# Optimization experiments

Hardware: AMD Instinct MI355X
Metric: run time of the kernel (lower is better)

The kernel has to match this reference:

```python
import jax, jax.numpy as jnp
import numpy as np

NUM_NODES = 50000
NUM_EDGES = 800000
INPUT_DIM = 128
HIDDEN_DIM = 128
PE_DIM = 64


def setup_inputs() -> dict:
    key = jax.random.key(0)
    ks = jax.random.split(key, 12)
    x = jax.random.normal(ks[0], (NUM_NODES, INPUT_DIM), dtype=jnp.float32)
    edge_index = jax.random.randint(ks[1], (2, NUM_EDGES), 0, NUM_NODES, dtype=jnp.int64)
    edge_pe = jax.random.normal(ks[2], (NUM_EDGES, PE_DIM), dtype=jnp.float32)
    # message_net: Linear(input+pe -> hidden), ReLU, Linear(hidden -> hidden)
    s1 = 1.0 / np.sqrt(INPUT_DIM + PE_DIM)
    W1 = jax.random.uniform(ks[3], (INPUT_DIM + PE_DIM, HIDDEN_DIM), minval=-s1, maxval=s1)
    b1 = jax.random.uniform(ks[4], (HIDDEN_DIM,), minval=-s1, maxval=s1)
    s2 = 1.0 / np.sqrt(HIDDEN_DIM)
    W2 = jax.random.uniform(ks[5], (HIDDEN_DIM, HIDDEN_DIM), minval=-s2, maxval=s2)
    b2 = jax.random.uniform(ks[6], (HIDDEN_DIM,), minval=-s2, maxval=s2)
    # update_net: Linear(input+hidden -> hidden), ReLU, Linear(hidden -> input)
    s3 = 1.0 / np.sqrt(INPUT_DIM + HIDDEN_DIM)
    U1 = jax.random.uniform(ks[7], (INPUT_DIM + HIDDEN_DIM, HIDDEN_DIM), minval=-s3, maxval=s3)
    c1 = jax.random.uniform(ks[8], (HIDDEN_DIM,), minval=-s3, maxval=s3)
    U2 = jax.random.uniform(ks[9], (HIDDEN_DIM, INPUT_DIM), minval=-s2, maxval=s2)
    c2 = jax.random.uniform(ks[10], (INPUT_DIM,), minval=-s2, maxval=s2)
    return {"x": x, "edge_pe": edge_pe, "W1": W1, "b1": b1, "W2": W2, "b2": b2,
            "U1": U1, "c1": c1, "U2": U2, "c2": c2, "edge_index": edge_index}


def reference(x, edge_pe, W1, b1, W2, b2, U1, c1, U2, c2, edge_index):
    src, dst = edge_index[0], edge_index[1]
    # gather source node features per edge: [E, input_dim]
    msg_in = jnp.concatenate([x[src], edge_pe], axis=-1)  # [E, input+pe]
    h = jax.nn.relu(msg_in @ W1 + b1)
    messages = h @ W2 + b2  # [E, hidden]
    # scatter-add messages to destination nodes
    aggregated = jax.ops.segment_sum(messages, dst, num_segments=x.shape[0])  # [N, hidden]
    upd_in = jnp.concatenate([x, aggregated], axis=-1)  # [N, input+hidden]
    u = jax.nn.relu(upd_in @ U1 + c1)
    return u @ U2 + c2  # [N, input_dim]
```

## Files before the change

kernel.cpp:

```cpp
#include <hip/hip_runtime.h>

#define NN 50000
#define NE 800000

typedef __attribute__((ext_vector_type(8))) short bf16x8;
typedef __attribute__((ext_vector_type(4))) float f32x4;

#define SWS(s, kt) ((s) ^ (((s) >> 3) & 6) ^ ((kt) & 3))

__device__ __forceinline__ unsigned short f2bf(float f) {
    union { float f; unsigned u; } v; v.f = f;
    unsigned r = v.u + 0x7FFFu + ((v.u >> 16) & 1u);
    return (unsigned short)(r >> 16);
}

__device__ __forceinline__ uint2 pack4(float a, float b, float c, float d) {
    uint2 p;
    p.x = (unsigned)f2bf(a) | ((unsigned)f2bf(b) << 16);
    p.y = (unsigned)f2bf(c) | ((unsigned)f2bf(d) << 16);
    return p;
}

__global__ void prep_weights(const float* __restrict__ W1, const float* __restrict__ W2,
                             const float* __restrict__ U1, const float* __restrict__ U2,
                             unsigned short* __restrict__ ws) {
    int tid = blockIdx.x * blockDim.x + threadIdx.x;
    const float* src; unsigned short* dst; int K;
    if (tid < 6144)        { src = W1; dst = ws;         K = 192; }
    else if (tid < 10240)  { tid -= 6144;  src = W2; dst = ws + 24576; K = 128; }
    else if (tid < 18432)  { tid -= 10240; src = U1; dst = ws + 40960; K = 256; }
    else if (tid < 22528)  { tid -= 18432; src = U2; dst = ws + 73728; K = 128; }
    else return;
    const int m = tid & 127, k = (tid >> 7) * 4;
    const int KT = K >> 5;
    uint2 p = pack4(src[(k + 0) * 128 + m], src[(k + 1) * 128 + m],
                    src[(k + 2) * 128 + m], src[(k + 3) * 128 + m]);
    const int mt = m >> 4, kt = k >> 5, lane = (m & 15) + (((k & 31) >> 3) << 4);
    const int off = (((mt * KT + kt) << 9) + (lane << 3) + ((k & 4) ? 4 : 0));
    *reinterpret_cast<uint2*>(dst + off) = p;
}

__global__ void prep_x(const float* __restrict__ x, unsigned short* __restrict__ xb) {
    const int i = (blockIdx.x * blockDim.x + threadIdx.x) * 8;
    if (i >= NN * 128) return;
    const float4 a = *reinterpret_cast<const float4*>(&x[i]);
    const float4 b = *reinterpret_cast<const float4*>(&x[i + 4]);
    const uint2 p0 = pack4(a.x, a.y, a.z, a.w);
    const uint2 p1 = pack4(b.x, b.y, b.z, b.w);
    *reinterpret_cast<uint4*>(&xb[i]) = make_uint4(p0.x, p0.y, p1.x, p1.y);
}

__global__ void hist_kernel(const int* __restrict__ ei, int* __restrict__ counts) {
    const int e = blockIdx.x * blockDim.x + threadIdx.x;
    if (e < NE) atomicAdd(&counts[ei[NE + e]], 1);
}

__global__ __launch_bounds__(256)
void scan1_kernel(const int* __restrict__ counts, int* __restrict__ offs,
                  int* __restrict__ bsums) {
    __shared__ int wsum[4];
    const int t = threadIdx.x, lane = t & 63, w = t >> 6;
    const int i = blockIdx.x * 256 + t;
    const int v = (i < NN) ? counts[i] : 0;
    int s = v;
#pragma unroll
    for (int d = 1; d < 64; d <<= 1) {
        int u = __shfl_up(s, d, 64);
        if (lane >= d) s += u;
    }
    if (lane == 63) wsum[w] = s;
    __syncthreads();
    if (t == 0) {
        int a = 0;
#pragma unroll
        for (int k = 0; k < 4; ++k) { int tmp = wsum[k]; wsum[k] = a; a += tmp; }
    }
    __syncthreads();
    const int excl = wsum[w] + s - v;
    if (i < NN) offs[i] = excl;
    if (t == 255) bsums[blockIdx.x] = wsum[3] + s;
}

__global__ __launch_bounds__(256)
void scan2_kernel(const int* __restrict__ bsums, int* __restrict__ boffs) {
    __shared__ int wsum[4];
    const int t = threadIdx.x, lane = t & 63, w = t >> 6;
    const int v = (t < 196) ? bsums[t] : 0;
    int s = v;
#pragma unroll
    for (int d = 1; d < 64; d <<= 1) {
        int u = __shfl_up(s, d, 64);
        if (lane >= d) s += u;
    }
    if (lane == 63) wsum[w] = s;
    __syncthreads();
    if (t == 0) {
        int a = 0;
#pragma unroll
        for (int k = 0; k < 4; ++k) { int tmp = wsum[k]; wsum[k] = a; a += tmp; }
    }
    __syncthreads();
    boffs[t] = wsum[w] + s - v;
}

__global__ __launch_bounds__(256)
void scan3_kernel(int* __restrict__ offs, const int* __restrict__ boffs,
                  int* __restrict__ cursor) {
    const int i = blockIdx.x * 256 + threadIdx.x;
    if (i < NN) {
        const int o = offs[i] + boffs[i >> 8];
        offs[i] = o;
        cursor[i] = o;
    }
}

__global__ void fill_kernel(const int* __restrict__ ei, int* __restrict__ cursor,
                            int* __restrict__ csrpos) {
    const int e = blockIdx.x * blockDim.x + threadIdx.x;
    if (e < NE) csrpos[e] = atomicAdd(&cursor[ei[NE + e]], 1);
}

template <int XBF>
__global__ __launch_bounds__(512)
void edge_kernel2(const float* __restrict__ x,
                  const unsigned short* __restrict__ xb,
                  const float* __restrict__ pe,
                  const float* __restrict__ b1,
                  const float* __restrict__ b2,
                  const int* __restrict__ ei,
                  const int* __restrict__ csrpos,
                  const unsigned short* __restrict__ wf,
                  unsigned short* __restrict__ msg)
{
    __shared__ __align__(16) unsigned char Asw[24576];
    __shared__ __align__(16) unsigned char Hsw[16384];

    const int t = threadIdx.x;
    const int l = t & 63;
    const int w = t >> 6;
    const int g = l >> 4;

    bf16x8 w1r[6], w2r[4];
    {
        const bf16x8* wp1 = reinterpret_cast<const bf16x8*>(wf);
        const bf16x8* wp2 = reinterpret_cast<const bf16x8*>(wf + 24576);
#pragma unroll
        for (int kt = 0; kt < 6; ++kt) w1r[kt] = wp1[(w * 6 + kt) * 64 + l];
#pragma unroll
        for (int kt = 0; kt < 4; ++kt) w2r[kt] = wp2[(w * 4 + kt) * 64 + l];
    }
    const float4 b1v = *reinterpret_cast<const float4*>(&b1[16 * w + 4 * g]);
    const float4 b2v = *reinterpret_cast<const float4*>(&b2[16 * w + 4 * g]);

    const int le = t >> 3;
    const int sub = t & 7;
    const int nt_s = le >> 4;
    const int lane_s = (le & 15) + ((sub & 3) << 4);

    uint4  rxb[2];
    float4 rxf[4];
    float4 rpf[2];

    const int tile0 = blockIdx.x * 5;

    {
        const int e0 = tile0 * 64;
        const int src = ei[e0 + le];
        if constexpr (XBF) {
#pragma unroll
            for (int j = 0; j < 2; ++j)
                rxb[j] = *reinterpret_cast<const uint4*>(&xb[(size_t)src * 128 + sub * 8 + 64 * j]);
        } else {
#pragma unroll
            for (int j = 0; j < 2; ++j) {
                rxf[2 * j]     = *reinterpret_cast<const float4*>(&x[(size_t)src * 128 + sub * 8 + 64 * j]);
                rxf[2 * j + 1] = *reinterpret_cast<const float4*>(&x[(size_t)src * 128 + sub * 8 + 64 * j + 4]);
            }
        }
        rpf[0] = *reinterpret_cast<const float4*>(&pe[(size_t)(e0 + le) * 64 + sub * 8]);
        rpf[1] = *reinterpret_cast<const float4*>(&pe[(size_t)(e0 + le) * 64 + sub * 8 + 4]);
    }

    for (int ti = 0; ti < 5; ++ti) {
        const int e0 = (tile0 + ti) * 64;
        int cp[4];
#pragma unroll
        for (int nt = 0; nt < 4; ++nt) cp[nt] = csrpos[e0 + nt * 16 + (l & 15)];

        __syncthreads();

        {
#pragma unroll
            for (int j = 0; j < 2; ++j) {
                const int kt = (sub >> 2) + 2 * j;
                uint4 v;
                if constexpr (XBF) v = rxb[j];
                else {
                    const uint2 p0 = pack4(rxf[2 * j].x, rxf[2 * j].y, rxf[2 * j].z, rxf[2 * j].w);
                    const uint2 p1 = pack4(rxf[2 * j + 1].x, rxf[2 * j + 1].y, rxf[2 * j + 1].z, rxf[2 * j + 1].w);
                    v = make_uint4(p0.x, p0.y, p1.x, p1.y);
                }
                *reinterpret_cast<uint4*>(Asw + ((kt * 4 + nt_s) << 10) + (SWS(lane_s, kt) << 4)) = v;
            }
            const int ktp = 4 + (sub >> 2);
            const uint2 q0 = pack4(rpf[0].x, rpf[0].y, rpf[0].z, rpf[0].w);
            const uint2 q1 = pack4(rpf[1].x, rpf[1].y, rpf[1].z, rpf[1].w);
            *reinterpret_cast<uint4*>(Asw + ((ktp * 4 + nt_s) << 10) + (SWS(lane_s, ktp) << 4)) =
                make_uint4(q0.x, q0.y, q1.x, q1.y);
        }

        if (ti < 4) {
            const int e0n = e0 + 64;
            const int srcn = ei[e0n + le];
            if constexpr (XBF) {
#pragma unroll
                for (int j = 0; j < 2; ++j)
                    rxb[j] = *reinterpret_cast<const uint4*>(&xb[(size_t)srcn * 128 + sub * 8 + 64 * j]);
            } else {
#pragma unroll
                for (int j = 0; j < 2; ++j) {
                    rxf[2 * j]     = *reinterpret_cast<const float4*>(&x[(size_t)srcn * 128 + sub * 8 + 64 * j]);
                    rxf[2 * j + 1] = *reinterpret_cast<const float4*>(&x[(size_t)srcn * 128 + sub * 8 + 64 * j + 4]);
                }
            }
            rpf[0] = *reinterpret_cast<const float4*>(&pe[(size_t)(e0n + le) * 64 + sub * 8]);
            rpf[1] = *reinterpret_cast<const float4*>(&pe[(size_t)(e0n + le) * 64 + sub * 8 + 4]);
        }

        __syncthreads();

        f32x4 acc[4];
#pragma unroll
        for (int nt = 0; nt < 4; ++nt) acc[nt] = (f32x4){0.f, 0.f, 0.f, 0.f};
#pragma unroll
        for (int kt = 0; kt < 6; ++kt) {
#pragma unroll
            for (int nt = 0; nt < 4; ++nt) {
                const bf16x8 af = *reinterpret_cast<const bf16x8*>(
                    Asw + ((kt * 4 + nt) << 10) + (SWS(l, kt) << 4));
                acc[nt] = __builtin_amdgcn_mfma_f32_16x16x32_bf16(w1r[kt], af, acc[nt], 0, 0, 0);
            }
        }

        {
            const int kt2 = (16 * w + 4 * g) >> 5;
            const int lane2 = (l & 15) + ((2 * (w & 1) + (g >> 1)) << 4);
            const int bo = (g & 1) << 3;
#pragma unroll
            for (int nt = 0; nt < 4; ++nt) {
                float v0 = fmaxf(acc[nt][0] + b1v.x, 0.f);
                float v1 = fmaxf(acc[nt][1] + b1v.y, 0.f);
                float v2 = fmaxf(acc[nt][2] + b1v.z, 0.f);
                float v3 = fmaxf(acc[nt][3] + b1v.w, 0.f);
                *reinterpret_cast<uint2*>(Hsw + ((kt2 * 4 + nt) << 10) + (SWS(lane2, kt2) << 4) + bo) =
                    pack4(v0, v1, v2, v3);
            }
        }

        __syncthreads();

#pragma unroll
        for (int nt = 0; nt < 4; ++nt) acc[nt] = (f32x4){0.f, 0.f, 0.f, 0.f};
#pragma unroll
        for (int kt = 0; kt < 4; ++kt) {
#pragma unroll
            for (int nt = 0; nt < 4; ++nt) {
                const bf16x8 hf = *reinterpret_cast<const bf16x8*>(
                    Hsw + ((kt * 4 + nt) << 10) + (SWS(l, kt) << 4));
                acc[nt] = __builtin_amdgcn_mfma_f32_16x16x32_bf16(w2r[kt], hf, acc[nt], 0, 0, 0);
            }
        }

        const int mbase = 16 * w + 4 * g;
#pragma unroll
        for (int nt = 0; nt < 4; ++nt) {
            *reinterpret_cast<uint2*>(&msg[(size_t)cp[nt] * 128 + mbase]) =
                pack4(acc[nt][0] + b2v.x, acc[nt][1] + b2v.y,
                      acc[nt][2] + b2v.z, acc[nt][3] + b2v.w);
        }
    }
}

template <int XBF>
__global__ __launch_bounds__(512)
void node_fused(const float* __restrict__ x,
                const unsigned short* __restrict__ xb,
                const float* __restrict__ c1,
                const float* __restrict__ c2,
                const unsigned short* __restrict__ wf,
                const int* __restrict__ offs,
                const int* __restrict__ counts,
                const unsigned short* __restrict__ msg,
                float* __restrict__ out)
{
    __shared__ __align__(16) unsigned char Asw[32768];
    __shared__ __align__(16) unsigned char Hsw[16384];

    const int t = threadIdx.x;
    const int l = t & 63;
    const int w = t >> 6;
    const int g = l >> 4;

    bf16x8 u1r[8], u2r[4];
    {
        const bf16x8* up1 = reinterpret_cast<const bf16x8*>(wf + 40960);
        const bf16x8* up2 = reinterpret_cast<const bf16x8*>(wf + 73728);
#pragma unroll
        for (int kt = 0; kt < 8; ++kt) u1r[kt] = up1[(w * 8 + kt) * 64 + l];
#pragma unroll
        for (int kt = 0; kt < 4; ++kt) u2r[kt] = up2[(w * 4 + kt) * 64 + l];
    }
    const float4 c1v = *reinterpret_cast<const float4*>(&c1[16 * w + 4 * g]);
    const float4 c2v = *reinterpret_cast<const float4*>(&c2[16 * w + 4 * g]);

    const int n0 = blockIdx.x * 64;
    const int le = t >> 3;
    const int q  = t & 7;
    const int nt_s = le >> 4;
    const int node = n0 + le;
    const bool valid = node < NN;

    float a16[16];
#pragma unroll
    for (int i = 0; i < 16; ++i) a16[i] = 0.f;
    int start = 0, cnt = 0;
    if (valid) { start = offs[node]; cnt = counts[node]; }
    for (int j = 0; j < cnt; ++j) {
        const uint4* mp = reinterpret_cast<const uint4*>(&msg[(size_t)(start + j) * 128 + q * 16]);
        const uint4 u0 = mp[0], u1 = mp[1];
        const unsigned arr[8] = {u0.x, u0.y, u0.z, u0.w, u1.x, u1.y, u1.z, u1.w};
#pragma unroll
        for (int r = 0; r < 8; ++r) {
            union { unsigned u; float f; } lo, hi;
            lo.u = arr[r] << 16;
            hi.u = arr[r] & 0xFFFF0000u;
            a16[2 * r]     += lo.f;
            a16[2 * r + 1] += hi.f;
        }
    }

#pragma unroll
    for (int i = 0; i < 2; ++i) {
        const int o = 2 * q + i;
        const int kt = o >> 2;
        const int slot = (le & 15) + ((o & 3) << 4);
        uint4 v = make_uint4(0u, 0u, 0u, 0u);
        if (valid) {
            if constexpr (XBF) {
                v = *reinterpret_cast<const uint4*>(&xb[(size_t)node * 128 + o * 8]);
            } else {
                const float4 f0 = *reinterpret_cast<const float4*>(&x[(size_t)node * 128 + o * 8]);
                const float4 f1 = *reinterpret_cast<const float4*>(&x[(size_t)node * 128 + o * 8 + 4]);
                const uint2 p0 = pack4(f0.x, f0.y, f0.z, f0.w);
                const uint2 p1 = pack4(f1.x, f1.y, f1.z, f1.w);
                v = make_uint4(p0.x, p0.y, p1.x, p1.y);
            }
        }
        *reinterpret_cast<uint4*>(Asw + ((kt * 4 + nt_s) << 10) + (SWS(slot, kt) << 4)) = v;
    }

    {
        const int kt = 4 + (q >> 1);
#pragma unroll
        for (int i = 0; i < 2; ++i) {
            const int j4 = 2 * (q & 1) + i;
            const int slot = (le & 15) + (j4 << 4);
            const uint2 p0 = pack4(a16[8 * i + 0], a16[8 * i + 1], a16[8 * i + 2], a16[8 * i + 3]);
            const uint2 p1 = pack4(a16[8 * i + 4], a16[8 * i + 5], a16[8 * i + 6], a16[8 * i + 7]);
            *reinterpret_cast<uint4*>(Asw + ((kt * 4 + nt_s) << 10) + (SWS(slot, kt) << 4)) =
                make_uint4(p0.x, p0.y, p1.x, p1.y);
        }
    }
    __syncthreads();

    f32x4 acc[4];
#pragma unroll
    for (int nt = 0; nt < 4; ++nt) acc[nt] = (f32x4){0.f, 0.f, 0.f, 0.f};
#pragma unroll
    for (int kt = 0; kt < 8; ++kt) {
#pragma unroll
        for (int nt = 0; nt < 4; ++nt) {
            const bf16x8 af = *reinterpret_cast<const bf16x8*>(
                Asw + ((kt * 4 + nt) << 10) + (SWS(l, kt) << 4));
            acc[nt] = __builtin_amdgcn_mfma_f32_16x16x32_bf16(u1r[kt], af, acc[nt], 0, 0, 0);
        }
    }

    {
        const int kt2 = (16 * w + 4 * g) >> 5;
        const int lane2 = (l & 15) + ((2 * (w & 1) + (g >> 1)) << 4);
        const int bo = (g & 1) << 3;
#pragma unroll
        for (int nt = 0; nt < 4; ++nt) {
            float v0 = fmaxf(acc[nt][0] + c1v.x, 0.f);
            float v1 = fmaxf(acc[nt][1] + c1v.y, 0.f);
            float v2 = fmaxf(acc[nt][2] + c1v.z, 0.f);
            float v3 = fmaxf(acc[nt][3] + c1v.w, 0.f);
            *reinterpret_cast<uint2*>(Hsw + ((kt2 * 4 + nt) << 10) + (SWS(lane2, kt2) << 4) + bo) =
                pack4(v0, v1, v2, v3);
        }
    }
    __syncthreads();

    f32x4 a2[4];
#pragma unroll
    for (int nt = 0; nt < 4; ++nt) a2[nt] = (f32x4){0.f, 0.f, 0.f, 0.f};
#pragma unroll
    for (int kt = 0; kt < 4; ++kt) {
#pragma unroll
        for (int nt = 0; nt < 4; ++nt) {
            const bf16x8 hf = *reinterpret_cast<const bf16x8*>(
                Hsw + ((kt * 4 + nt) << 10) + (SWS(l, kt) << 4));
            a2[nt] = __builtin_amdgcn_mfma_f32_16x16x32_bf16(u2r[kt], hf, a2[nt], 0, 0, 0);
        }
    }

    const int mbase = 16 * w + 4 * g;
#pragma unroll
    for (int nt = 0; nt < 4; ++nt) {
        const int n = n0 + nt * 16 + (l & 15);
        if (n < NN) {
            float4 o;
            o.x = a2[nt][0] + c2v.x;
            o.y = a2[nt][1] + c2v.y;
            o.z = a2[nt][2] + c2v.z;
            o.w = a2[nt][3] + c2v.w;
            *reinterpret_cast<float4*>(&out[(size_t)n * 128 + mbase]) = o;
        }
    }
}

__global__ __launch_bounds__(256)
void edge_atomic(const float* __restrict__ x, const float* __restrict__ pe,
                 const float* __restrict__ b1, const float* __restrict__ b2,
                 const int* __restrict__ ei, const unsigned short* __restrict__ wf,
                 float* __restrict__ agg)
{
    __shared__ __align__(16) unsigned char smem[24576 + 16384];
    unsigned char* Asw = smem;
    unsigned char* Hsw = smem + 24576;

    const int t = threadIdx.x;
    const int l = t & 63;
    const int w = t >> 6;
    const int g = l >> 4;

    bf16x8 w1r[2][6], w2r[2][4];
    {
        const bf16x8* wp1 = reinterpret_cast<const bf16x8*>(wf);
        const bf16x8* wp2 = reinterpret_cast<const bf16x8*>(wf + 24576);
#pragma unroll
        for (int dm = 0; dm < 2; ++dm) {
            const int mt = 2 * w + dm;
#pragma unroll
            for (int kt = 0; kt < 6; ++kt) w1r[dm][kt] = wp1[(mt * 6 + kt) * 64 + l];
#pragma unroll
            for (int kt = 0; kt < 4; ++kt) w2r[dm][kt] = wp2[(mt * 4 + kt) * 64 + l];
        }
    }
    float4 b1v[2], b2v[2];
#pragma unroll
    for (int dm = 0; dm < 2; ++dm) {
        b1v[dm] = *reinterpret_cast<const float4*>(&b1[32 * w + 16 * dm + 4 * g]);
        b2v[dm] = *reinterpret_cast<const float4*>(&b2[32 * w + 16 * dm + 4 * g]);
    }

    const int le = t >> 2;
    const int lq = (t & 3) * 4;
    const int nt_s = le >> 4;

    for (int tile = blockIdx.x * 5; tile < blockIdx.x * 5 + 5; ++tile) {
        const int e0 = tile * 64;
        const int src = ei[e0 + le];
#pragma unroll
        for (int j = 0; j < 12; ++j) {
            const int k = lq + 16 * j;
            float4 av;
            if (j < 8) av = *reinterpret_cast<const float4*>(&x[(size_t)src * 128 + k]);
            else       av = *reinterpret_cast<const float4*>(&pe[(size_t)(e0 + le) * 64 + (k - 128)]);
            const int kt = k >> 5;
            const int lane = (le & 15) + (((k & 31) >> 3) << 4);
            const int off = ((kt * 4 + nt_s) << 10) + (lane << 4) + ((k & 4) << 1);
            *reinterpret_cast<uint2*>(Asw + off) = pack4(av.x, av.y, av.z, av.w);
        }
        int dstv[4];
#pragma unroll
        for (int nt = 0; nt < 4; ++nt) dstv[nt] = ei[NE + e0 + nt * 16 + (l & 15)];
        __syncthreads();

        f32x4 acc[2][4];
#pragma unroll
        for (int dm = 0; dm < 2; ++dm)
#pragma unroll
            for (int nt = 0; nt < 4; ++nt) acc[dm][nt] = (f32x4){0.f, 0.f, 0.f, 0.f};
#pragma unroll
        for (int kt = 0; kt < 6; ++kt) {
#pragma unroll
            for (int nt = 0; nt < 4; ++nt) {
                const bf16x8 af = *reinterpret_cast<const bf16x8*>(Asw + ((kt * 4 + nt) << 10) + (l << 4));
                acc[0][nt] = __builtin_amdgcn_mfma_f32_16x16x32_bf16(w1r[0][kt], af, acc[0][nt], 0, 0, 0);
                acc[1][nt] = __builtin_amdgcn_mfma_f32_16x16x32_bf16(w1r[1][kt], af, acc[1][nt], 0, 0, 0);
            }
        }
#pragma unroll
        for (int dm = 0; dm < 2; ++dm) {
            const float bb[4] = {b1v[dm].x, b1v[dm].y, b1v[dm].z, b1v[dm].w};
            const int lane2 = (l & 15) + ((2 * dm + (g >> 1)) << 4);
#pragma unroll
            for (int nt = 0; nt < 4; ++nt) {
                float v0 = fmaxf(acc[dm][nt][0] + bb[0], 0.f);
                float v1 = fmaxf(acc[dm][nt][1] + bb[1], 0.f);
                float v2 = fmaxf(acc[dm][nt][2] + bb[2], 0.f);
                float v3 = fmaxf(acc[dm][nt][3] + bb[3], 0.f);
                const int off = ((w * 4 + nt) << 10) + (lane2 << 4) + ((g & 1) << 3);
                *reinterpret_cast<uint2*>(Hsw + off) = pack4(v0, v1, v2, v3);
            }
        }
        __syncthreads();

        f32x4 acc2[2][4];
#pragma unroll
        for (int dm = 0; dm < 2; ++dm)
#pragma unroll
            for (int nt = 0; nt < 4; ++nt) acc2[dm][nt] = (f32x4){0.f, 0.f, 0.f, 0.f};
#pragma unroll
        for (int kt = 0; kt < 4; ++kt) {
#pragma unroll
            for (int nt = 0; nt < 4; ++nt) {
                const bf16x8 hf = *reinterpret_cast<const bf16x8*>(Hsw + ((kt * 4 + nt) << 10) + (l << 4));
                acc2[0][nt] = __builtin_amdgcn_mfma_f32_16x16x32_bf16(w2r[0][kt], hf, acc2[0][nt], 0, 0, 0);
                acc2[1][nt] = __builtin_amdgcn_mfma_f32_16x16x32_bf16(w2r[1][kt], hf, acc2[1][nt], 0, 0, 0);
            }
        }
#pragma unroll
        for (int dm = 0; dm < 2; ++dm) {
            const float bb[4] = {b2v[dm].x, b2v[dm].y, b2v[dm].z, b2v[dm].w};
            const int mbase = 32 * w + 16 * dm + 4 * g;
#pragma unroll
            for (int nt = 0; nt < 4; ++nt) {
                float* ap = &agg[(size_t)dstv[nt] * 128 + mbase];
                atomicAdd(ap + 0, acc2[dm][nt][0] + bb[0]);
                atomicAdd(ap + 1, acc2[dm][nt][1] + bb[1]);
                atomicAdd(ap + 2, acc2[dm][nt][2] + bb[2]);
                atomicAdd(ap + 3, acc2[dm][nt][3] + bb[3]);
            }
        }
    }
}

__global__ __launch_bounds__(256)
void node_legacy(const float* __restrict__ x,
                 const float* __restrict__ c1,
                 const float* __restrict__ c2,
                 const unsigned short* __restrict__ wf,
                 float* __restrict__ out)
{
    __shared__ __align__(16) unsigned char smem[32768 + 16384];
    unsigned char* Asw = smem;
    unsigned char* Hsw = smem + 32768;

    const int t = threadIdx.x;
    const int l = t & 63;
    const int w = t >> 6;
    const int g = l >> 4;

    bf16x8 u1r[2][8], u2r[2][4];
    {
        const bf16x8* up1 = reinterpret_cast<const bf16x8*>(wf + 40960);
        const bf16x8* up2 = reinterpret_cast<const bf16x8*>(wf + 73728);
#pragma unroll
        for (int dm = 0; dm < 2; ++dm) {
            const int mt = 2 * w + dm;
#pragma unroll
            for (int kt = 0; kt < 8; ++kt) u1r[dm][kt] = up1[(mt * 8 + kt) * 64 + l];
#pragma unroll
            for (int kt = 0; kt < 4; ++kt) u2r[dm][kt] = up2[(mt * 4 + kt) * 64 + l];
        }
    }
    float4 c1v[2], c2v[2];
#pragma unroll
    for (int dm = 0; dm < 2; ++dm) {
        c1v[dm] = *reinterpret_cast<const float4*>(&c1[32 * w + 16 * dm + 4 * g]);
        c2v[dm] = *reinterpret_cast<const float4*>(&c2[32 * w + 16 * dm + 4 * g]);
    }

    const int n0 = blockIdx.x * 64;
    const int le = t >> 2;
    const int lq = (t & 3) * 4;
    const int nt_s = le >> 4;
    const int node = n0 + le;
    const bool valid = node < NN;

#pragma unroll
    for (int j = 0; j < 16; ++j) {
        const int k = lq + 16 * j;
        float4 av = make_float4(0.f, 0.f, 0.f, 0.f);
        if (valid) {
            if (j < 8) av = *reinterpret_cast<const float4*>(&x[(size_t)node * 128 + k]);
            else       av = *reinterpret_cast<const float4*>(&out[(size_t)node * 128 + (k - 128)]);
        }
        const int kt = k >> 5;
        const int lane = (le & 15) + (((k & 31) >> 3) << 4);
        const int off = ((kt * 4 + nt_s) << 10) + (lane << 4) + ((k & 4) << 1);
        *reinterpret_cast<uint2*>(Asw + off) = pack4(av.x, av.y, av.z, av.w);
    }
    __syncthreads();

    f32x4 acc[2][4];
#pragma unroll
    for (int dm = 0; dm < 2; ++dm)
#pragma unroll
        for (int nt = 0; nt < 4; ++nt) acc[dm][nt] = (f32x4){0.f, 0.f, 0.f, 0.f};
#pragma unroll
    for (int kt = 0; kt < 8; ++kt) {
        bf16x8 af[4];
#pragma unroll
        for (int nt = 0; nt < 4; ++nt)
            af[nt] = *reinterpret_cast<const bf16x8*>(Asw + ((kt * 4 + nt) << 10) + (l << 4));
#pragma unroll
        for (int nt = 0; nt < 4; ++nt) {
            acc[0][nt] = __builtin_amdgcn_mfma_f32_16x16x32_bf16(u1r[0][kt], af[nt], acc[0][nt], 0, 0, 0);
            acc[1][nt] = __builtin_amdgcn_mfma_f32_16x16x32_bf16(u1r[1][kt], af[nt], acc[1][nt], 0, 0, 0);
        }
    }

#pragma unroll
    for (int dm = 0; dm < 2; ++dm) {
        const float bb[4] = {c1v[dm].x, c1v[dm].y, c1v[dm].z, c1v[dm].w};
        const int lane2 = (l & 15) + ((2 * dm + (g >> 1)) << 4);
#pragma unroll
        for (int nt = 0; nt < 4; ++nt) {
            float v0 = fmaxf(acc[dm][nt][0] + bb[0], 0.f);
            float v1 = fmaxf(acc[dm][nt][1] + bb[1], 0.f);
            float v2 = fmaxf(acc[dm][nt][2] + bb[2], 0.f);
            float v3 = fmaxf(acc[dm][nt][3] + bb[3], 0.f);
            const int off = ((w * 4 + nt) << 10) + (lane2 << 4) + ((g & 1) << 3);
            *reinterpret_cast<uint2*>(Hsw + off) = pack4(v0, v1, v2, v3);
        }
    }
    __syncthreads();

    f32x4 acc2[2][4];
#pragma unroll
    for (int dm = 0; dm < 2; ++dm)
#pragma unroll
        for (int nt = 0; nt < 4; ++nt) acc2[dm][nt] = (f32x4){0.f, 0.f, 0.f, 0.f};
#pragma unroll
    for (int kt = 0; kt < 4; ++kt) {
        bf16x8 hf[4];
#pragma unroll
        for (int nt = 0; nt < 4; ++nt)
            hf[nt] = *reinterpret_cast<const bf16x8*>(Hsw + ((kt * 4 + nt) << 10) + (l << 4));
#pragma unroll
        for (int nt = 0; nt < 4; ++nt) {
            acc2[0][nt] = __builtin_amdgcn_mfma_f32_16x16x32_bf16(u2r[0][kt], hf[nt], acc2[0][nt], 0, 0, 0);
            acc2[1][nt] = __builtin_amdgcn_mfma_f32_16x16x32_bf16(u2r[1][kt], hf[nt], acc2[1][nt], 0, 0, 0);
        }
    }

#pragma unroll
    for (int dm = 0; dm < 2; ++dm) {
        const int mbase = 32 * w + 16 * dm + 4 * g;
#pragma unroll
        for (int nt = 0; nt < 4; ++nt) {
            const int n = n0 + nt * 16 + (l & 15);
            if (n < NN) {
                float4 o;
                o.x = acc2[dm][nt][0] + c2v[dm].x;
                o.y = acc2[dm][nt][1] + c2v[dm].y;
                o.z = acc2[dm][nt][2] + c2v[dm].z;
                o.w = acc2[dm][nt][3] + c2v[dm].w;
                *reinterpret_cast<float4*>(&out[(size_t)n * 128 + mbase]) = o;
            }
        }
    }
}

extern "C" void kernel_launch(void* const* d_in, const int* in_sizes, int n_in,
                              void* d_out, int out_size, void* d_ws, size_t ws_size,
                              hipStream_t stream) {
    const float* x  = (const float*)d_in[0];
    const float* pe = (const float*)d_in[1];
    const float* W1 = (const float*)d_in[2];
    const float* b1 = (const float*)d_in[3];
    const float* W2 = (const float*)d_in[4];
    const float* b2 = (const float*)d_in[5];
    const float* U1 = (const float*)d_in[6];
    const float* c1 = (const float*)d_in[7];
    const float* U2 = (const float*)d_in[8];
    const float* c2 = (const float*)d_in[9];
    const int*   ei = (const int*)d_in[10];
    float* out = (float*)d_out;

    const size_t MB = 1 << 20;
    unsigned short* wf = (unsigned short*)d_ws;
    int* counts = (int*)((char*)d_ws + 1 * MB);
    int* offs   = (int*)((char*)d_ws + 1 * MB + 256 * 1024);
    int* cursor = (int*)((char*)d_ws + 1 * MB + 512 * 1024);
    int* bsums  = (int*)((char*)d_ws + 1 * MB + 768 * 1024);
    int* boffs  = (int*)((char*)d_ws + 1 * MB + 772 * 1024);
    int* csrpos = (int*)((char*)d_ws + 2 * MB);
    unsigned short* xb   = (unsigned short*)((char*)d_ws + 6 * MB);
    unsigned short* msgA = (unsigned short*)((char*)d_ws + 19 * MB);
    unsigned short* msgB = (unsigned short*)((char*)d_ws + 6 * MB);

    const size_t MSG_BYTES = (size_t)NE * 128 * 2;
    const size_t REQA = 19 * MB + MSG_BYTES;
    const size_t REQB = 6 * MB + MSG_BYTES;

    prep_weights<<<88, 256, 0, stream>>>(W1, W2, U1, U2, wf);

    if (ws_size >= REQB) {
        const bool tierA = ws_size >= REQA;
        unsigned short* msg = tierA ? msgA : msgB;

        hipMemsetAsync(counts, 0, 50176 * sizeof(int), stream);
        if (tierA) prep_x<<<3125, 256, 0, stream>>>(x, xb);
        hist_kernel<<<NE / 256, 256, 0, stream>>>(ei, counts);
        scan1_kernel<<<196, 256, 0, stream>>>(counts, offs, bsums);
        scan2_kernel<<<1, 256, 0, stream>>>(bsums, boffs);
        scan3_kernel<<<196, 256, 0, stream>>>(offs, boffs, cursor);
        fill_kernel<<<NE / 256, 256, 0, stream>>>(ei, cursor, csrpos);
        if (tierA) {
            edge_kernel2<1><<<NE / 64 / 5, 512, 0, stream>>>(x, xb, pe, b1, b2, ei, csrpos, wf, msg);
            node_fused<1><<<(NN + 63) / 64, 512, 0, stream>>>(x, xb, c1, c2, wf, offs, counts, msg, out);
        } else {
            edge_kernel2<0><<<NE / 64 / 5, 512, 0, stream>>>(x, nullptr, pe, b1, b2, ei, csrpos, wf, msg);
            node_fused<0><<<(NN + 63) / 64, 512, 0, stream>>>(x, nullptr, c1, c2, wf, offs, counts, msg, out);
        }
    } else {
        hipMemsetAsync(out, 0, (size_t)NN * 128 * sizeof(float), stream);
        edge_atomic<<<NE / 64 / 5, 256, 0, stream>>>(x, pe, b1, b2, ei, wf, out);
        node_legacy<<<(NN + 63) / 64, 256, 0, stream>>>(x, c1, c2, wf, out);
    }
}
```

Baseline: 288.0 us.

## Halve edge-kernel waves with two M-tiles per wave and use hardware bf16 packing

```diff
diff --git a/kernel.cpp b/kernel.cpp
--- a/kernel.cpp
+++ b/kernel.cpp
@@ -8,17 +8,13 @@
 
 #define SWS(s, kt) ((s) ^ (((s) >> 3) & 6) ^ ((kt) & 3))
 
-__device__ __forceinline__ unsigned short f2bf(float f) {
-    union { float f; unsigned u; } v; v.f = f;
-    unsigned r = v.u + 0x7FFFu + ((v.u >> 16) & 1u);
-    return (unsigned short)(r >> 16);
-}
-
+__device__ __forceinline__ unsigned cvtpk(float lo, float hi) {
+    unsigned r;
+    asm("v_cvt_pk_bf16_f32 %0, %1, %2" : "=v"(r) : "v"(lo), "v"(hi));
+    return r;
+}
 __device__ __forceinline__ uint2 pack4(float a, float b, float c, float d) {
-    uint2 p;
-    p.x = (unsigned)f2bf(a) | ((unsigned)f2bf(b) << 16);
-    p.y = (unsigned)f2bf(c) | ((unsigned)f2bf(d) << 16);
-    return p;
+    return make_uint2(cvtpk(a, b), cvtpk(c, d));
 }
 
 __global__ void prep_weights(const float* __restrict__ W1, const float* __restrict__ W2,
@@ -121,8 +117,8 @@
 }
 
 template <int XBF>
-__global__ __launch_bounds__(512)
-void edge_kernel2(const float* __restrict__ x,
+__global__ __launch_bounds__(256, 3)
+void edge_kernel3(const float* __restrict__ x,
                   const unsigned short* __restrict__ xb,
                   const float* __restrict__ pe,
                   const float* __restrict__ b1,
@@ -140,45 +136,44 @@
     const int w = t >> 6;
     const int g = l >> 4;
 
-    bf16x8 w1r[6], w2r[4];
+    bf16x8 w1r[2][6], w2r[2][4];
     {
         const bf16x8* wp1 = reinterpret_cast<const bf16x8*>(wf);
         const bf16x8* wp2 = reinterpret_cast<const bf16x8*>(wf + 24576);
 #pragma unroll
-        for (int kt = 0; kt < 6; ++kt) w1r[kt] = wp1[(w * 6 + kt) * 64 + l];
-#pragma unroll
-        for (int kt = 0; kt < 4; ++kt) w2r[kt] = wp2[(w * 4 + kt) * 64 + l];
-    }
-    const float4 b1v = *reinterpret_cast<const float4*>(&b1[16 * w + 4 * g]);
-    const float4 b2v = *reinterpret_cast<const float4*>(&b2[16 * w + 4 * g]);
-
-    const int le = t >> 3;
-    const int sub = t & 7;
+        for (int dm = 0; dm < 2; ++dm) {
+            const int mt = 2 * w + dm;
+#pragma unroll
+            for (int kt = 0; kt < 6; ++kt) w1r[dm][kt] = wp1[(mt * 6 + kt) * 64 + l];
+#pragma unroll
+            for (int kt = 0; kt < 4; ++kt) w2r[dm][kt] = wp2[(mt * 4 + kt) * 64 + l];
+        }
+    }
+    float4 b1v[2], b2v[2];
+#pragma unroll
+    for (int dm = 0; dm < 2; ++dm) {
+        b1v[dm] = *reinterpret_cast<const float4*>(&b1[32 * w + 16 * dm + 4 * g]);
+        b2v[dm] = *reinterpret_cast<const float4*>(&b2[32 * w + 16 * dm + 4 * g]);
+    }
+
+    const int le = t >> 2;
+    const int sub = t & 3;
     const int nt_s = le >> 4;
-    const int lane_s = (le & 15) + ((sub & 3) << 4);
-
-    uint4  rxb[2];
-    float4 rxf[4];
-    float4 rpf[2];
+
+    uint4  rxb[4];
+    float4 rpf[4];
 
     const int tile0 = blockIdx.x * 5;
 
-    {
+    if constexpr (XBF) {
         const int e0 = tile0 * 64;
         const int src = ei[e0 + le];
-        if constexpr (XBF) {
-#pragma unroll
-            for (int j = 0; j < 2; ++j)
-                rxb[j] = *reinterpret_cast<const uint4*>(&xb[(size_t)src * 128 + sub * 8 + 64 * j]);
-        } else {
-#pragma unroll
-            for (int j = 0; j < 2; ++j) {
-                rxf[2 * j]     = *reinterpret_cast<const float4*>(&x[(size_t)src * 128 + sub * 8 + 64 * j]);
-                rxf[2 * j + 1] = *reinterpret_cast<const float4*>(&x[(size_t)src * 128 + sub * 8 + 64 * j + 4]);
-            }
-        }
-        rpf[0] = *reinterpret_cast<const float4*>(&pe[(size_t)(e0 + le) * 64 + sub * 8]);
-        rpf[1] = *reinterpret_cast<const float4*>(&pe[(size_t)(e0 + le) * 64 + sub * 8 + 4]);
+#pragma unroll
+        for (int i = 0; i < 4; ++i)
+            rxb[i] = *reinterpret_cast<const uint4*>(&xb[(size_t)src * 128 + 32 * sub + 8 * i]);
+#pragma unroll
+        for (int q = 0; q < 4; ++q)
+            rpf[q] = *reinterpret_cast<const float4*>(&pe[(size_t)(e0 + le) * 64 + 16 * sub + 4 * q]);
     }
 
     for (int ti = 0; ti < 5; ++ti) {
@@ -189,94 +184,118 @@
 
         __syncthreads();
 
-        {
-#pragma unroll
-            for (int j = 0; j < 2; ++j) {
-                const int kt = (sub >> 2) + 2 * j;
-                uint4 v;
-                if constexpr (XBF) v = rxb[j];
-                else {
-                    const uint2 p0 = pack4(rxf[2 * j].x, rxf[2 * j].y, rxf[2 * j].z, rxf[2 * j].w);
-                    const uint2 p1 = pack4(rxf[2 * j + 1].x, rxf[2 * j + 1].y, rxf[2 * j + 1].z, rxf[2 * j + 1].w);
-                    v = make_uint4(p0.x, p0.y, p1.x, p1.y);
-                }
-                *reinterpret_cast<uint4*>(Asw + ((kt * 4 + nt_s) << 10) + (SWS(lane_s, kt) << 4)) = v;
-            }
-            const int ktp = 4 + (sub >> 2);
-            const uint2 q0 = pack4(rpf[0].x, rpf[0].y, rpf[0].z, rpf[0].w);
-            const uint2 q1 = pack4(rpf[1].x, rpf[1].y, rpf[1].z, rpf[1].w);
-            *reinterpret_cast<uint4*>(Asw + ((ktp * 4 + nt_s) << 10) + (SWS(lane_s, ktp) << 4)) =
-                make_uint4(q0.x, q0.y, q1.x, q1.y);
-        }
-
-        if (ti < 4) {
+        if constexpr (XBF) {
+#pragma unroll
+            for (int i = 0; i < 4; ++i) {
+                const int slot = (le & 15) + (i << 4);
+                *reinterpret_cast<uint4*>(Asw + ((sub * 4 + nt_s) << 10) + (SWS(slot, sub) << 4)) = rxb[i];
+            }
+#pragma unroll
+            for (int i2 = 0; i2 < 2; ++i2) {
+                const int p = 2 * sub + i2;
+                const int kt = 4 + (p >> 2);
+                const int slot = (le & 15) + ((p & 3) << 4);
+                const float4 f0 = rpf[2 * i2], f1 = rpf[2 * i2 + 1];
+                *reinterpret_cast<uint4*>(Asw + ((kt * 4 + nt_s) << 10) + (SWS(slot, kt) << 4)) =
+                    make_uint4(cvtpk(f0.x, f0.y), cvtpk(f0.z, f0.w),
+                               cvtpk(f1.x, f1.y), cvtpk(f1.z, f1.w));
+            }
+        } else {
+            const int src = ei[e0 + le];
+#pragma unroll
+            for (int i = 0; i < 4; ++i) {
+                const float4 f0 = *reinterpret_cast<const float4*>(&x[(size_t)src * 128 + 32 * sub + 8 * i]);
+                const float4 f1 = *reinterpret_cast<const float4*>(&x[(size_t)src * 128 + 32 * sub + 8 * i + 4]);
+                const int slot = (le & 15) + (i << 4);
+                *reinterpret_cast<uint4*>(Asw + ((sub * 4 + nt_s) << 10) + (SWS(slot, sub) << 4)) =
+                    make_uint4(cvtpk(f0.x, f0.y), cvtpk(f0.z, f0.w),
+                               cvtpk(f1.x, f1.y), cvtpk(f1.z, f1.w));
+            }
+#pragma unroll
+            for (int i2 = 0; i2 < 2; ++i2) {
+                const int p = 2 * sub + i2;
+                const int kt = 4 + (p >> 2);
+                const int slot = (le & 15) + ((p & 3) << 4);
+                const float4 f0 = *reinterpret_cast<const float4*>(&pe[(size_t)(e0 + le) * 64 + 8 * p]);
+                const float4 f1 = *reinterpret_cast<const float4*>(&pe[(size_t)(e0 + le) * 64 + 8 * p + 4]);
+                *reinterpret_cast<uint4*>(Asw + ((kt * 4 + nt_s) << 10) + (SWS(slot, kt) << 4)) =
+                    make_uint4(cvtpk(f0.x, f0.y), cvtpk(f0.z, f0.w),
+                               cvtpk(f1.x, f1.y), cvtpk(f1.z, f1.w));
+            }
+        }
+
+        if (XBF && ti < 4) {
             const int e0n = e0 + 64;
             const int srcn = ei[e0n + le];
-            if constexpr (XBF) {
-#pragma unroll
-                for (int j = 0; j < 2; ++j)
-                    rxb[j] = *reinterpret_cast<const uint4*>(&xb[(size_t)srcn * 128 + sub * 8 + 64 * j]);
-            } else {
-#pragma unroll
-                for (int j = 0; j < 2; ++j) {
-                    rxf[2 * j]     = *reinterpret_cast<const float4*>(&x[(size_t)srcn * 128 + sub * 8 + 64 * j]);
-                    rxf[2 * j + 1] = *reinterpret_cast<const float4*>(&x[(size_t)srcn * 128 + sub * 8 + 64 * j + 4]);
-                }
-            }
-            rpf[0] = *reinterpret_cast<const float4*>(&pe[(size_t)(e0n + le) * 64 + sub * 8]);
-            rpf[1] = *reinterpret_cast<const float4*>(&pe[(size_t)(e0n + le) * 64 + sub * 8 + 4]);
+#pragma unroll
+            for (int i = 0; i < 4; ++i)
+                rxb[i] = *reinterpret_cast<const uint4*>(&xb[(size_t)srcn * 128 + 32 * sub + 8 * i]);
+#pragma unroll
+            for (int q = 0; q < 4; ++q)
+                rpf[q] = *reinterpret_cast<const float4*>(&pe[(size_t)(e0n + le) * 64 + 16 * sub + 4 * q]);
         }
 
         __syncthreads();
 
-        f32x4 acc[4];
-#pragma unroll
-        for (int nt = 0; nt < 4; ++nt) acc[nt] = (f32x4){0.f, 0.f, 0.f, 0.f};
+        f32x4 acc[2][4];
+#pragma unroll
+        for (int dm = 0; dm < 2; ++dm)
+#pragma unroll
+            for (int nt = 0; nt < 4; ++nt) acc[dm][nt] = (f32x4){0.f, 0.f, 0.f, 0.f};
 #pragma unroll
         for (int kt = 0; kt < 6; ++kt) {
 #pragma unroll
             for (int nt = 0; nt < 4; ++nt) {
                 const bf16x8 af = *reinterpret_cast<const bf16x8*>(
                     Asw + ((kt * 4 + nt) << 10) + (SWS(l, kt) << 4));
-                acc[nt] = __builtin_amdgcn_mfma_f32_16x16x32_bf16(w1r[kt], af, acc[nt], 0, 0, 0);
+                acc[0][nt] = __builtin_amdgcn_mfma_f32_16x16x32_bf16(w1r[0][kt], af, acc[0][nt], 0, 0, 0);
+                acc[1][nt] = __builtin_amdgcn_mfma_f32_16x16x32_bf16(w1r[1][kt], af, acc[1][nt], 0, 0, 0);
             }
         }
 
         {
-            const int kt2 = (16 * w + 4 * g) >> 5;
-            const int lane2 = (l & 15) + ((2 * (w & 1) + (g >> 1)) << 4);
-            const int bo = (g & 1) << 3;
-#pragma unroll
-            for (int nt = 0; nt < 4; ++nt) {
-                float v0 = fmaxf(acc[nt][0] + b1v.x, 0.f);
-                float v1 = fmaxf(acc[nt][1] + b1v.y, 0.f);
-                float v2 = fmaxf(acc[nt][2] + b1v.z, 0.f);
-                float v3 = fmaxf(acc[nt][3] + b1v.w, 0.f);
-                *reinterpret_cast<uint2*>(Hsw + ((kt2 * 4 + nt) << 10) + (SWS(lane2, kt2) << 4) + bo) =
-                    pack4(v0, v1, v2, v3);
+#pragma unroll
+            for (int dm = 0; dm < 2; ++dm) {
+                const int lane2 = (l & 15) + ((2 * dm + (g >> 1)) << 4);
+                const int bo = (g & 1) << 3;
+#pragma unroll
+                for (int nt = 0; nt < 4; ++nt) {
+                    float v0 = fmaxf(acc[dm][nt][0] + b1v[dm].x, 0.f);
+                    float v1 = fmaxf(acc[dm][nt][1] + b1v[dm].y, 0.f);
+                    float v2 = fmaxf(acc[dm][nt][2] + b1v[dm].z, 0.f);
+                    float v3 = fmaxf(acc[dm][nt][3] + b1v[dm].w, 0.f);
+                    *reinterpret_cast<uint2*>(Hsw + ((w * 4 + nt) << 10) + (SWS(lane2, w) << 4) + bo) =
+                        make_uint2(cvtpk(v0, v1), cvtpk(v2, v3));
+                }
             }
         }
 
         __syncthreads();
 
 #pragma unroll
-        for (int nt = 0; nt < 4; ++nt) acc[nt] = (f32x4){0.f, 0.f, 0.f, 0.f};
+        for (int dm = 0; dm < 2; ++dm)
+#pragma unroll
+            for (int nt = 0; nt < 4; ++nt) acc[dm][nt] = (f32x4){0.f, 0.f, 0.f, 0.f};
 #pragma unroll
         for (int kt = 0; kt < 4; ++kt) {
 #pragma unroll
             for (int nt = 0; nt < 4; ++nt) {
                 const bf16x8 hf = *reinterpret_cast<const bf16x8*>(
                     Hsw + ((kt * 4 + nt) << 10) + (SWS(l, kt) << 4));
-                acc[nt] = __builtin_amdgcn_mfma_f32_16x16x32_bf16(w2r[kt], hf, acc[nt], 0, 0, 0);
-            }
-        }
-
-        const int mbase = 16 * w + 4 * g;
-#pragma unroll
-        for (int nt = 0; nt < 4; ++nt) {
-            *reinterpret_cast<uint2*>(&msg[(size_t)cp[nt] * 128 + mbase]) =
-                pack4(acc[nt][0] + b2v.x, acc[nt][1] + b2v.y,
-                      acc[nt][2] + b2v.z, acc[nt][3] + b2v.w);
+                acc[0][nt] = __builtin_amdgcn_mfma_f32_16x16x32_bf16(w2r[0][kt], hf, acc[0][nt], 0, 0, 0);
+                acc[1][nt] = __builtin_amdgcn_mfma_f32_16x16x32_bf16(w2r[1][kt], hf, acc[1][nt], 0, 0, 0);
+            }
+        }
+
+#pragma unroll
+        for (int dm = 0; dm < 2; ++dm) {
+            const int mbase = 32 * w + 16 * dm + 4 * g;
+#pragma unroll
+            for (int nt = 0; nt < 4; ++nt) {
+                *reinterpret_cast<uint2*>(&msg[(size_t)cp[nt] * 128 + mbase]) =
+                    make_uint2(cvtpk(acc[dm][nt][0] + b2v[dm].x, acc[dm][nt][1] + b2v[dm].y),
+                               cvtpk(acc[dm][nt][2] + b2v[dm].z, acc[dm][nt][3] + b2v[dm].w));
+            }
         }
     }
 }
@@ -351,9 +370,8 @@
             } else {
                 const float4 f0 = *reinterpret_cast<const float4*>(&x[(size_t)node * 128 + o * 8]);
                 const float4 f1 = *reinterpret_cast<const float4*>(&x[(size_t)node * 128 + o * 8 + 4]);
-                const uint2 p0 = pack4(f0.x, f0.y, f0.z, f0.w);
-                const uint2 p1 = pack4(f1.x, f1.y, f1.z, f1.w);
-                v = make_uint4(p0.x, p0.y, p1.x, p1.y);
+                v = make_uint4(cvtpk(f0.x, f0.y), cvtpk(f0.z, f0.w),
+                               cvtpk(f1.x, f1.y), cvtpk(f1.z, f1.w));
             }
         }
         *reinterpret_cast<uint4*>(Asw + ((kt * 4 + nt_s) << 10) + (SWS(slot, kt) << 4)) = v;
@@ -365,10 +383,9 @@
         for (int i = 0; i < 2; ++i) {
             const int j4 = 2 * (q & 1) + i;
             const int slot = (le & 15) + (j4 << 4);
-            const uint2 p0 = pack4(a16[8 * i + 0], a16[8 * i + 1], a16[8 * i + 2], a16[8 * i + 3]);
-            const uint2 p1 = pack4(a16[8 * i + 4], a16[8 * i + 5], a16[8 * i + 6], a16[8 * i + 7]);
             *reinterpret_cast<uint4*>(Asw + ((kt * 4 + nt_s) << 10) + (SWS(slot, kt) << 4)) =
-                make_uint4(p0.x, p0.y, p1.x, p1.y);
+                make_uint4(cvtpk(a16[8 * i + 0], a16[8 * i + 1]), cvtpk(a16[8 * i + 2], a16[8 * i + 3]),
+                           cvtpk(a16[8 * i + 4], a16[8 * i + 5]), cvtpk(a16[8 * i + 6], a16[8 * i + 7]));
         }
     }
     __syncthreads();
@@ -397,7 +414,7 @@
             float v2 = fmaxf(acc[nt][2] + c1v.z, 0.f);
             float v3 = fmaxf(acc[nt][3] + c1v.w, 0.f);
             *reinterpret_cast<uint2*>(Hsw + ((kt2 * 4 + nt) << 10) + (SWS(lane2, kt2) << 4) + bo) =
-                pack4(v0, v1, v2, v3);
+                make_uint2(cvtpk(v0, v1), cvtpk(v2, v3));
         }
     }
     __syncthreads();
@@ -722,10 +739,10 @@
         scan3_kernel<<<196, 256, 0, stream>>>(offs, boffs, cursor);
         fill_kernel<<<NE / 256, 256, 0, stream>>>(ei, cursor, csrpos);
         if (tierA) {
-            edge_kernel2<1><<<NE / 64 / 5, 512, 0, stream>>>(x, xb, pe, b1, b2, ei, csrpos, wf, msg);
+            edge_kernel3<1><<<NE / 64 / 5, 256, 0, stream>>>(x, xb, pe, b1, b2, ei, csrpos, wf, msg);
             node_fused<1><<<(NN + 63) / 64, 512, 0, stream>>>(x, xb, c1, c2, wf, offs, counts, msg, out);
         } else {
-            edge_kernel2<0><<<NE / 64 / 5, 512, 0, stream>>>(x, nullptr, pe, b1, b2, ei, csrpos, wf, msg);
+            edge_kernel3<0><<<NE / 64 / 5, 256, 0, stream>>>(x, nullptr, pe, b1, b2, ei, csrpos, wf, msg);
             node_fused<0><<<(NN + 63) / 64, 512, 0, stream>>>(x, nullptr, c1, c2, wf, offs, counts, msg, out);
         }
     } else {
```

Result: slower. 400.9 us (+39.2%).
